# Kernel optimization log

Hardware: AMD Instinct MI355X
Metric: run time of the kernel (lower is better)

The kernel has to match this reference:

```python
import jax, jax.numpy as jnp
import numpy as np


def _prelu(x, p):
    # PReLU with a single learnable slope (torch default num_parameters=1)
    return jnp.where(x >= 0, x, p[0] * x)


def setup_inputs() -> dict:
    key = jax.random.key(0)
    ks = jax.random.split(key, 8)
    B, R, N, S, Din, Dout = 8, 4, 2048, 6, 32, 32
    return {
        "theta_param": jax.random.uniform(ks[0], (R, S), dtype=jnp.float32),
        "t_param": jax.random.uniform(ks[1], (R, S), dtype=jnp.float32),
        "a_input_batched": jax.random.uniform(ks[2], (B, R, N, N), dtype=jnp.float32),
        "x_input_batched": jax.random.normal(ks[3], (B, R, N, Din), dtype=jnp.float32),
        "fc_w": jax.random.normal(ks[4], (R, Din, Dout), dtype=jnp.float32) * 0.05,
        "fc_b": jax.random.normal(ks[5], (R, Dout), dtype=jnp.float32) * 0.05,
        "conv_w": jax.random.normal(ks[6], (R, R), dtype=jnp.float32) * 0.05,
        "conv_b": jax.random.normal(ks[7], (R,), dtype=jnp.float32) * 0.05,
        "prelu0": jnp.full((1,), 0.25, dtype=jnp.float32),
        "prelu1": jnp.full((1,), 0.25, dtype=jnp.float32),
    }


def reference(theta_param, t_param, a_input_batched, x_input_batched,
              fc_w, fc_b, conv_w, conv_b, prelu0, prelu1):
    # The inner diffusion-step loop is sum_s theta[r,s]*t[r,s] -> scalar per relation.
    coef = jnp.sum(theta_param * t_param, axis=1)              # [R]
    # diffusion_mat = coef[r] * A[b,r]; fold the scalar into the matmul result.
    diff_feat = jnp.einsum('brnm,brmd->brnd', a_input_batched, x_input_batched)
    diff_feat = coef[None, :, None, None] * diff_feat          # [B,R,N,Din]
    # Per-relation linear layer.
    fc_out = jnp.einsum('brnd,rde->brne', diff_feat, fc_w) + fc_b[None, :, None, :]
    h = _prelu(fc_out, prelu0)                                 # activation0
    # 1x1 Conv2d over the relation channel == [R,R] mixing matrix + bias.
    mixed = jnp.einsum('brne,qr->bqne', h, conv_w) + conv_b[None, :, None, None]
    latent = _prelu(mixed, prelu1)                             # activation1
    return latent  # original returns (latent, latent) — same tensor twice
```

## Files before the change

kernel.cpp:

```cpp
#include <hip/hip_runtime.h>
#include <hip/hip_bf16.h>

typedef __attribute__((ext_vector_type(8))) short  bf16x8;
typedef __attribute__((ext_vector_type(4))) float  f32x4;
typedef __attribute__((ext_vector_type(4))) int    i32x4;
typedef __attribute__((address_space(3))) void       as3void;
typedef const __attribute__((address_space(1))) void as1void;

#define B_   8
#define R_   4
#define N_   2048
#define S_   6
#define DIN  32
#define DOUT 32
#define NT   16

__global__ __launch_bounds__(256) void prep_xw(
    const float* __restrict__ theta, const float* __restrict__ tpar,
    const float* __restrict__ X,     const float* __restrict__ fcw,
    __hip_bfloat16* __restrict__ xwt)
{
    int br    = blockIdx.x >> 5;
    int mtile = blockIdx.x & 31;
    int r     = br & 3;
    int t     = threadIdx.x;
    int m     = mtile * 64 + (t & 63);
    int egrp  = t >> 6;

    float coef = 0.f;
#pragma unroll
    for (int s = 0; s < S_; ++s) coef += theta[r * S_ + s] * tpar[r * S_ + s];

    const float* xrow = X + ((size_t)br * N_ + m) * DIN;
    float xr[DIN];
#pragma unroll
    for (int i = 0; i < DIN / 4; ++i) {
        f32x4 v = *(const f32x4*)(xrow + i * 4);
        xr[i * 4 + 0] = v.x; xr[i * 4 + 1] = v.y;
        xr[i * 4 + 2] = v.z; xr[i * 4 + 3] = v.w;
    }
#pragma unroll
    for (int eb = 0; eb < 8; ++eb) {
        int e = egrp * 8 + eb;
        float acc = 0.f;
#pragma unroll
        for (int d = 0; d < DIN; ++d) acc += xr[d] * fcw[(r * DIN + d) * DOUT + e];
        xwt[((size_t)br * DOUT + e) * N_ + m] = __float2bfloat16(coef * acc);
    }
}

__global__ __launch_bounds__(256) void fused_main(
    const float* __restrict__ A,   const __hip_bfloat16* __restrict__ xwt,
    const float* __restrict__ fcb, const float* __restrict__ cw,
    const float* __restrict__ cb,  const float* __restrict__ p0p,
    const float* __restrict__ p1p, float* __restrict__ out)
{
    __shared__ char smem[65536];

    int b    = blockIdx.x >> 7;
    int tile = blockIdx.x & 127;
    int n0   = tile * 16;
    int t    = threadIdx.x;
    int r    = t >> 6;
    int l    = t & 63;
    int row16 = l & 15;
    int kg    = l >> 4;
    int swzr  = (row16 & 7) << 4;
    int ldsbase = r * 8192;
    int hl   = l >> 5;
    int l31  = l & 31;

    const char* Ab = (const char*)(A + (((size_t)(b * R_ + r)) * N_ + n0) * N_);
    const char* srcp[8];
#pragma unroll
    for (int i = 0; i < 8; ++i) {
        int row = 2 * i + hl;
        srcp[i] = Ab + (size_t)row * (N_ * 4) + ((l31 * 16) ^ ((row & 7) << 4));
    }

    const ushort* xw  = (const ushort*)xwt + (size_t)(b * R_ + r) * DOUT * N_;
    const ushort* bp0 = xw + (size_t)row16 * N_        + kg * 8;
    const ushort* bp1 = xw + (size_t)(16 + row16) * N_ + kg * 8;

#define STAGE_A(CUR, KT) do {                                                    \
    _Pragma("unroll")                                                            \
    for (int i_ = 0; i_ < 8; ++i_) {                                             \
        __builtin_amdgcn_global_load_lds(                                        \
            (as1void*)(srcp[i_] + (size_t)(KT) * 512),                           \
            (as3void*)&smem[(CUR) * 32768 + ldsbase + i_ * 1024], 16, 0, 0);     \
    } } while (0)

#define LOADB(P, KT) do {                                                        \
    asm volatile("global_load_dwordx4 %0, %1, off" : "=v"(P##0) : "v"(bp0 + (KT) * 128 +  0)); \
    asm volatile("global_load_dwordx4 %0, %1, off" : "=v"(P##1) : "v"(bp0 + (KT) * 128 + 32)); \
    asm volatile("global_load_dwordx4 %0, %1, off" : "=v"(P##2) : "v"(bp0 + (KT) * 128 + 64)); \
    asm volatile("global_load_dwordx4 %0, %1, off" : "=v"(P##3) : "v"(bp0 + (KT) * 128 + 96)); \
    asm volatile("global_load_dwordx4 %0, %1, off" : "=v"(P##4) : "v"(bp1 + (KT) * 128 +  0)); \
    asm volatile("global_load_dwordx4 %0, %1, off" : "=v"(P##5) : "v"(bp1 + (KT) * 128 + 32)); \
    asm volatile("global_load_dwordx4 %0, %1, off" : "=v"(P##6) : "v"(bp1 + (KT) * 128 + 64)); \
    asm volatile("global_load_dwordx4 %0, %1, off" : "=v"(P##7) : "v"(bp1 + (KT) * 128 + 96)); \
    } while (0)

    f32x4 acc0 = {0.f, 0.f, 0.f, 0.f};
    f32x4 acc1 = {0.f, 0.f, 0.f, 0.f};
    i32x4 bc0, bc1, bc2, bc3, bc4, bc5, bc6, bc7;
    i32x4 bn0, bn1, bn2, bn3, bn4, bn5, bn6, bn7;

    STAGE_A(0, 0);
    LOADB(bc, 0);

#pragma unroll 2
    for (int kt = 0; kt < NT; ++kt) {
        int cur = kt & 1;
        __builtin_amdgcn_sched_barrier(0);
        if (kt < NT - 1) {
            STAGE_A(cur ^ 1, kt + 1);
            LOADB(bn, kt + 1);
            __builtin_amdgcn_sched_barrier(0);
            asm volatile("s_waitcnt vmcnt(16)" ::: "memory");
        } else {
            __builtin_amdgcn_sched_barrier(0);
            asm volatile("s_waitcnt vmcnt(0)" ::: "memory");
        }
        __builtin_amdgcn_sched_barrier(0);

        {
            const char* abuf = &smem[cur * 32768 + ldsbase];
            int rbase = row16 * 512;
#define KSTEP(KS, BA, BB) do {                                                   \
    f32x4 lo = *(const f32x4*)(abuf + rbase + (((KS) * 128 + kg * 32 +  0) ^ swzr)); \
    f32x4 hi = *(const f32x4*)(abuf + rbase + (((KS) * 128 + kg * 32 + 16) ^ swzr)); \
    i32x4 av;                                                                    \
    asm("v_cvt_pk_bf16_f32 %0, %1, %2" : "=v"(av.x) : "v"(lo.x), "v"(lo.y));     \
    asm("v_cvt_pk_bf16_f32 %0, %1, %2" : "=v"(av.y) : "v"(lo.z), "v"(lo.w));     \
    asm("v_cvt_pk_bf16_f32 %0, %1, %2" : "=v"(av.z) : "v"(hi.x), "v"(hi.y));     \
    asm("v_cvt_pk_bf16_f32 %0, %1, %2" : "=v"(av.w) : "v"(hi.z), "v"(hi.w));     \
    bf16x8 af = __builtin_bit_cast(bf16x8, av);                                  \
    acc0 = __builtin_amdgcn_mfma_f32_16x16x32_bf16(af, __builtin_bit_cast(bf16x8, BA), acc0, 0, 0, 0); \
    acc1 = __builtin_amdgcn_mfma_f32_16x16x32_bf16(af, __builtin_bit_cast(bf16x8, BB), acc1, 0, 0, 0); \
    } while (0)
            KSTEP(0, bc0, bc4);
            KSTEP(1, bc1, bc5);
            KSTEP(2, bc2, bc6);
            KSTEP(3, bc3, bc7);
#undef KSTEP
        }
        bc0 = bn0; bc1 = bn1; bc2 = bn2; bc3 = bn3;
        bc4 = bn4; bc5 = bn5; bc6 = bn6; bc7 = bn7;
    }
#undef STAGE_A
#undef LOADB

    float p0 = p0p[0], p1 = p1p[0];

    __syncthreads();
    float (*hlds)[16][DOUT + 1] = (float (*)[16][DOUT + 1])(void*)smem;
#pragma unroll
    for (int j = 0; j < 4; ++j) {
        int rw = kg * 4 + j;
        float v0 = acc0[j] + fcb[r * DOUT + row16];
        float v1 = acc1[j] + fcb[r * DOUT + 16 + row16];
        hlds[r][rw][row16]      = v0 >= 0.f ? v0 : p0 * v0;
        hlds[r][rw][16 + row16] = v1 >= 0.f ? v1 : p0 * v1;
    }
    __syncthreads();

    int q = r;
    float c0 = cw[q * R_ + 0], c1 = cw[q * R_ + 1];
    float c2 = cw[q * R_ + 2], c3 = cw[q * R_ + 3];
    float cbq = cb[q];
    int e  = l & 31;
    int rg = l >> 5;
#pragma unroll
    for (int i = 0; i < 8; ++i) {
        int row = rg * 8 + i;
        float mx = cbq + c0 * hlds[0][row][e] + c1 * hlds[1][row][e]
                       + c2 * hlds[2][row][e] + c3 * hlds[3][row][e];
        float lat = mx >= 0.f ? mx : p1 * mx;
        out[(((size_t)b * R_ + q) * N_ + (n0 + row)) * DOUT + e] = lat;
    }
}

extern "C" void kernel_launch(void* const* d_in, const int* in_sizes, int n_in,
                              void* d_out, int out_size, void* d_ws, size_t ws_size,
                              hipStream_t stream)
{
    const float* theta = (const float*)d_in[0];
    const float* tpar  = (const float*)d_in[1];
    const float* A     = (const float*)d_in[2];
    const float* X     = (const float*)d_in[3];
    const float* fcw   = (const float*)d_in[4];
    const float* fcb   = (const float*)d_in[5];
    const float* cw    = (const float*)d_in[6];
    const float* cb    = (const float*)d_in[7];
    const float* p0    = (const float*)d_in[8];
    const float* p1    = (const float*)d_in[9];

    __hip_bfloat16* xwt = (__hip_bfloat16*)d_ws;

    prep_xw<<<B_ * R_ * (N_ / 64), 256, 0, stream>>>(theta, tpar, X, fcw, xwt);
    fused_main<<<B_ * (N_ / 16), 256, 0, stream>>>(A, xwt, fcb, cw, cb, p0, p1,
                                                   (float*)d_out);
}
```

Baseline: 138.6 us.

## Double row tile to 32 per block, halve K step, add block index swizzle

```diff
diff --git a/kernel.cpp b/kernel.cpp
--- a/kernel.cpp
+++ b/kernel.cpp
@@ -13,7 +13,7 @@
 #define S_   6
 #define DIN  32
 #define DOUT 32
-#define NT   16
+#define NT   32
 
 __global__ __launch_bounds__(256) void prep_xw(
     const float* __restrict__ theta, const float* __restrict__ tpar,
@@ -57,9 +57,11 @@
 {
     __shared__ char smem[65536];
 
-    int b    = blockIdx.x >> 7;
-    int tile = blockIdx.x & 127;
-    int n0   = tile * 16;
+    int bid  = blockIdx.x;
+    int swz  = (bid & 7) * 64 + (bid >> 3);
+    int b    = swz >> 6;
+    int tile = swz & 63;
+    int n0   = tile * 32;
     int t    = threadIdx.x;
     int r    = t >> 6;
     int l    = t & 63;
@@ -67,15 +69,13 @@
     int kg    = l >> 4;
     int swzr  = (row16 & 7) << 4;
     int ldsbase = r * 8192;
-    int hl   = l >> 5;
-    int l31  = l & 31;
 
     const char* Ab = (const char*)(A + (((size_t)(b * R_ + r)) * N_ + n0) * N_);
     const char* srcp[8];
 #pragma unroll
     for (int i = 0; i < 8; ++i) {
-        int row = 2 * i + hl;
-        srcp[i] = Ab + (size_t)row * (N_ * 4) + ((l31 * 16) ^ ((row & 7) << 4));
+        int row = 4 * i + (l >> 4);
+        srcp[i] = Ab + (size_t)row * (N_ * 4) + (((l & 15) * 16) ^ ((row & 7) << 4));
     }
 
     const ushort* xw  = (const ushort*)xwt + (size_t)(b * R_ + r) * DOUT * N_;
@@ -86,25 +86,20 @@
     _Pragma("unroll")                                                            \
     for (int i_ = 0; i_ < 8; ++i_) {                                             \
         __builtin_amdgcn_global_load_lds(                                        \
-            (as1void*)(srcp[i_] + (size_t)(KT) * 512),                           \
+            (as1void*)(srcp[i_] + (size_t)(KT) * 256),                           \
             (as3void*)&smem[(CUR) * 32768 + ldsbase + i_ * 1024], 16, 0, 0);     \
     } } while (0)
 
 #define LOADB(P, KT) do {                                                        \
-    asm volatile("global_load_dwordx4 %0, %1, off" : "=v"(P##0) : "v"(bp0 + (KT) * 128 +  0)); \
-    asm volatile("global_load_dwordx4 %0, %1, off" : "=v"(P##1) : "v"(bp0 + (KT) * 128 + 32)); \
-    asm volatile("global_load_dwordx4 %0, %1, off" : "=v"(P##2) : "v"(bp0 + (KT) * 128 + 64)); \
-    asm volatile("global_load_dwordx4 %0, %1, off" : "=v"(P##3) : "v"(bp0 + (KT) * 128 + 96)); \
-    asm volatile("global_load_dwordx4 %0, %1, off" : "=v"(P##4) : "v"(bp1 + (KT) * 128 +  0)); \
-    asm volatile("global_load_dwordx4 %0, %1, off" : "=v"(P##5) : "v"(bp1 + (KT) * 128 + 32)); \
-    asm volatile("global_load_dwordx4 %0, %1, off" : "=v"(P##6) : "v"(bp1 + (KT) * 128 + 64)); \
-    asm volatile("global_load_dwordx4 %0, %1, off" : "=v"(P##7) : "v"(bp1 + (KT) * 128 + 96)); \
+    asm volatile("global_load_dwordx4 %0, %1, off" : "=v"(P##0) : "v"(bp0 + (KT) * 64 +  0)); \
+    asm volatile("global_load_dwordx4 %0, %1, off" : "=v"(P##1) : "v"(bp0 + (KT) * 64 + 32)); \
+    asm volatile("global_load_dwordx4 %0, %1, off" : "=v"(P##2) : "v"(bp1 + (KT) * 64 +  0)); \
+    asm volatile("global_load_dwordx4 %0, %1, off" : "=v"(P##3) : "v"(bp1 + (KT) * 64 + 32)); \
     } while (0)
 
-    f32x4 acc0 = {0.f, 0.f, 0.f, 0.f};
-    f32x4 acc1 = {0.f, 0.f, 0.f, 0.f};
-    i32x4 bc0, bc1, bc2, bc3, bc4, bc5, bc6, bc7;
-    i32x4 bn0, bn1, bn2, bn3, bn4, bn5, bn6, bn7;
+    f32x4 acc00 = {0.f,0.f,0.f,0.f}, acc01 = {0.f,0.f,0.f,0.f};
+    f32x4 acc10 = {0.f,0.f,0.f,0.f}, acc11 = {0.f,0.f,0.f,0.f};
+    i32x4 bc0, bc1, bc2, bc3, bn0, bn1, bn2, bn3;
 
     STAGE_A(0, 0);
     LOADB(bc, 0);
@@ -117,7 +112,7 @@
             STAGE_A(cur ^ 1, kt + 1);
             LOADB(bn, kt + 1);
             __builtin_amdgcn_sched_barrier(0);
-            asm volatile("s_waitcnt vmcnt(16)" ::: "memory");
+            asm volatile("s_waitcnt vmcnt(12)" ::: "memory");
         } else {
             __builtin_amdgcn_sched_barrier(0);
             asm volatile("s_waitcnt vmcnt(0)" ::: "memory");
@@ -126,27 +121,32 @@
 
         {
             const char* abuf = &smem[cur * 32768 + ldsbase];
-            int rbase = row16 * 512;
 #define KSTEP(KS, BA, BB) do {                                                   \
-    f32x4 lo = *(const f32x4*)(abuf + rbase + (((KS) * 128 + kg * 32 +  0) ^ swzr)); \
-    f32x4 hi = *(const f32x4*)(abuf + rbase + (((KS) * 128 + kg * 32 + 16) ^ swzr)); \
-    i32x4 av;                                                                    \
-    asm("v_cvt_pk_bf16_f32 %0, %1, %2" : "=v"(av.x) : "v"(lo.x), "v"(lo.y));     \
-    asm("v_cvt_pk_bf16_f32 %0, %1, %2" : "=v"(av.y) : "v"(lo.z), "v"(lo.w));     \
-    asm("v_cvt_pk_bf16_f32 %0, %1, %2" : "=v"(av.z) : "v"(hi.x), "v"(hi.y));     \
-    asm("v_cvt_pk_bf16_f32 %0, %1, %2" : "=v"(av.w) : "v"(hi.z), "v"(hi.w));     \
-    bf16x8 af = __builtin_bit_cast(bf16x8, av);                                  \
-    acc0 = __builtin_amdgcn_mfma_f32_16x16x32_bf16(af, __builtin_bit_cast(bf16x8, BA), acc0, 0, 0, 0); \
-    acc1 = __builtin_amdgcn_mfma_f32_16x16x32_bf16(af, __builtin_bit_cast(bf16x8, BB), acc1, 0, 0, 0); \
+    f32x4 lo0 = *(const f32x4*)(abuf + (row16      ) * 256 + (((KS)*128 + kg*32 +  0) ^ swzr)); \
+    f32x4 hi0 = *(const f32x4*)(abuf + (row16      ) * 256 + (((KS)*128 + kg*32 + 16) ^ swzr)); \
+    f32x4 lo1 = *(const f32x4*)(abuf + (row16 + 16 ) * 256 + (((KS)*128 + kg*32 +  0) ^ swzr)); \
+    f32x4 hi1 = *(const f32x4*)(abuf + (row16 + 16 ) * 256 + (((KS)*128 + kg*32 + 16) ^ swzr)); \
+    i32x4 av0, av1;                                                              \
+    asm("v_cvt_pk_bf16_f32 %0, %1, %2" : "=v"(av0.x) : "v"(lo0.x), "v"(lo0.y));  \
+    asm("v_cvt_pk_bf16_f32 %0, %1, %2" : "=v"(av0.y) : "v"(lo0.z), "v"(lo0.w));  \
+    asm("v_cvt_pk_bf16_f32 %0, %1, %2" : "=v"(av0.z) : "v"(hi0.x), "v"(hi0.y));  \
+    asm("v_cvt_pk_bf16_f32 %0, %1, %2" : "=v"(av0.w) : "v"(hi0.z), "v"(hi0.w));  \
+    asm("v_cvt_pk_bf16_f32 %0, %1, %2" : "=v"(av1.x) : "v"(lo1.x), "v"(lo1.y));  \
+    asm("v_cvt_pk_bf16_f32 %0, %1, %2" : "=v"(av1.y) : "v"(lo1.z), "v"(lo1.w));  \
+    asm("v_cvt_pk_bf16_f32 %0, %1, %2" : "=v"(av1.z) : "v"(hi1.x), "v"(hi1.y));  \
+    asm("v_cvt_pk_bf16_f32 %0, %1, %2" : "=v"(av1.w) : "v"(hi1.z), "v"(hi1.w));  \
+    bf16x8 a0 = __builtin_bit_cast(bf16x8, av0);                                 \
+    bf16x8 a1 = __builtin_bit_cast(bf16x8, av1);                                 \
+    acc00 = __builtin_amdgcn_mfma_f32_16x16x32_bf16(a0, __builtin_bit_cast(bf16x8, BA), acc00, 0, 0, 0); \
+    acc01 = __builtin_amdgcn_mfma_f32_16x16x32_bf16(a0, __builtin_bit_cast(bf16x8, BB), acc01, 0, 0, 0); \
+    acc10 = __builtin_amdgcn_mfma_f32_16x16x32_bf16(a1, __builtin_bit_cast(bf16x8, BA), acc10, 0, 0, 0); \
+    acc11 = __builtin_amdgcn_mfma_f32_16x16x32_bf16(a1, __builtin_bit_cast(bf16x8, BB), acc11, 0, 0, 0); \
     } while (0)
-            KSTEP(0, bc0, bc4);
-            KSTEP(1, bc1, bc5);
-            KSTEP(2, bc2, bc6);
-            KSTEP(3, bc3, bc7);
+            KSTEP(0, bc0, bc2);
+            KSTEP(1, bc1, bc3);
 #undef KSTEP
         }
         bc0 = bn0; bc1 = bn1; bc2 = bn2; bc3 = bn3;
-        bc4 = bn4; bc5 = bn5; bc6 = bn6; bc7 = bn7;
     }
 #undef STAGE_A
 #undef LOADB
@@ -154,14 +154,18 @@
     float p0 = p0p[0], p1 = p1p[0];
 
     __syncthreads();
-    float (*hlds)[16][DOUT + 1] = (float (*)[16][DOUT + 1])(void*)smem;
+    float (*hlds)[32][DOUT + 1] = (float (*)[32][DOUT + 1])(void*)smem;
 #pragma unroll
     for (int j = 0; j < 4; ++j) {
         int rw = kg * 4 + j;
-        float v0 = acc0[j] + fcb[r * DOUT + row16];
-        float v1 = acc1[j] + fcb[r * DOUT + 16 + row16];
-        hlds[r][rw][row16]      = v0 >= 0.f ? v0 : p0 * v0;
-        hlds[r][rw][16 + row16] = v1 >= 0.f ? v1 : p0 * v1;
+        float fb0 = fcb[r * DOUT + row16];
+        float fb1 = fcb[r * DOUT + 16 + row16];
+        float v00 = acc00[j] + fb0, v01 = acc01[j] + fb1;
+        float v10 = acc10[j] + fb0, v11 = acc11[j] + fb1;
+        hlds[r][rw][row16]           = v00 >= 0.f ? v00 : p0 * v00;
+        hlds[r][rw][16 + row16]      = v01 >= 0.f ? v01 : p0 * v01;
+        hlds[r][16 + rw][row16]      = v10 >= 0.f ? v10 : p0 * v10;
+        hlds[r][16 + rw][16 + row16] = v11 >= 0.f ? v11 : p0 * v11;
     }
     __syncthreads();
 
@@ -170,10 +174,10 @@
     float c2 = cw[q * R_ + 2], c3 = cw[q * R_ + 3];
     float cbq = cb[q];
     int e  = l & 31;
-    int rg = l >> 5;
-#pragma unroll
-    for (int i = 0; i < 8; ++i) {
-        int row = rg * 8 + i;
+    int half = l >> 5;
+#pragma unroll
+    for (int i = 0; i < 16; ++i) {
+        int row = half * 16 + i;
         float mx = cbq + c0 * hlds[0][row][e] + c1 * hlds[1][row][e]
                        + c2 * hlds[2][row][e] + c3 * hlds[3][row][e];
         float lat = mx >= 0.f ? mx : p1 * mx;
@@ -199,6 +203,6 @@
     __hip_bfloat16* xwt = (__hip_bfloat16*)d_ws;
 
     prep_xw<<<B_ * R_ * (N_ / 64), 256, 0, stream>>>(theta, tpar, X, fcw, xwt);
-    fused_main<<<B_ * (N_ / 16), 256, 0, stream>>>(A, xwt, fcb, cw, cb, p0, p1,
+    fused_main<<<B_ * (N_ / 32), 256, 0, stream>>>(A, xwt, fcb, cw, cb, p0, p1,
                                                    (float*)d_out);
 }
```

Measured after the change: 206.0 us. 48.7% more time.
